# Kernel optimization log

Hardware: AMD Instinct MI355X
Metric: run time of the kernel (lower is better)

The kernel has to match this reference:

```python
import jax, jax.numpy as jnp
import numpy as np

N_HEAD = 12
LN_EPS = 1e-5


def setup_inputs() -> dict:
    key = jax.random.key(0)
    ks = jax.random.split(key, 4)
    B, T, C = 4, 2048, 768
    s = C ** -0.5
    return {
        "x": jax.random.normal(ks[0], (B, T, C), jnp.float32),
        "w_attn": jax.random.normal(ks[1], (C, 3 * C), jnp.float32) * s,
        "b_attn": jnp.zeros((3 * C,), jnp.float32),
        "w_proj": jax.random.normal(ks[2], (C, C), jnp.float32) * s,
        "b_proj": jnp.zeros((C,), jnp.float32),
        "ln1_g": jnp.ones((C,), jnp.float32),
        "ln1_b": jnp.zeros((C,), jnp.float32),
        "ln2_g": jnp.ones((C,), jnp.float32),
        "ln2_b": jnp.zeros((C,), jnp.float32),
    }


def _layernorm(x, g, b):
    mu = jnp.mean(x, axis=-1, keepdims=True)
    var = jnp.mean(jnp.square(x - mu), axis=-1, keepdims=True)
    return (x - mu) * jax.lax.rsqrt(var + LN_EPS) * g + b


def _attn(h, w_attn, b_attn, w_proj, b_proj):
    B, T, C = h.shape
    hd = C // N_HEAD
    # Faithful to torch: view(B,T,H,3*hd) then split 3*hd -> q,k,v per head
    qkv = (h @ w_attn + b_attn).reshape(B, T, N_HEAD, 3, hd)
    q = jnp.transpose(qkv[:, :, :, 0, :], (0, 2, 1, 3))  # (B,H,T,hd)
    k = jnp.transpose(qkv[:, :, :, 1, :], (0, 2, 1, 3))
    v = jnp.transpose(qkv[:, :, :, 2, :], (0, 2, 1, 3))
    # NOTE: scale is C**-0.5 (full embed dim) and there is NO causal mask,
    # exactly as in the source.
    scores = jnp.einsum("bhtd,bhsd->bhts", q, k) * (C ** -0.5)
    a = jax.nn.softmax(scores, axis=-1)
    y = jnp.einsum("bhts,bhsd->bhtd", a, v)
    y = jnp.transpose(y, (0, 2, 1, 3)).reshape(B, T, C)
    return y @ w_proj + b_proj


def reference(x, w_attn, b_attn, w_proj, b_proj, ln1_g, ln1_b, ln2_g, ln2_b):
    # Faithful to source Block.forward: attn applied twice, MLP never called.
    x = x + _attn(_layernorm(x, ln1_g, ln1_b), w_attn, b_attn, w_proj, b_proj)
    x = x + _attn(_layernorm(x, ln2_g, ln2_b), w_attn, b_attn, w_proj, b_proj)
    return x
```

## Files before the change

kernel.cpp:

```cpp
#include <hip/hip_runtime.h>


using bf16x8 = __attribute__((ext_vector_type(8))) short;
using f32x4  = __attribute__((ext_vector_type(4))) float;

__device__ __forceinline__ unsigned short f2b(float f) {
  unsigned u = __builtin_bit_cast(unsigned, f);
  u += 0x7FFFu + ((u >> 16) & 1u);
  return (unsigned short)(u >> 16);
}
__device__ __forceinline__ float b2f(unsigned short s) {
  return __builtin_bit_cast(float, (unsigned)s << 16);
}

#define ASYNC16(g, l)                                                        \
  __builtin_amdgcn_global_load_lds(                                          \
      (const __attribute__((address_space(1))) void*)(g),                    \
      (__attribute__((address_space(3))) void*)(l), 16, 0, 0)

__global__ __launch_bounds__(256) void wt_kernel(const float* __restrict__ w,
                                                 unsigned short* __restrict__ wt,
                                                 int N) {
  __shared__ float tile[32][33];
  const int n0 = blockIdx.x * 32, k0 = blockIdx.y * 32;
  const int tx = threadIdx.x, ty = threadIdx.y;
#pragma unroll
  for (int i = 0; i < 32; i += 8)
    tile[ty + i][tx] = w[(size_t)(k0 + ty + i) * N + n0 + tx];
  __syncthreads();
#pragma unroll
  for (int i = 0; i < 32; i += 8)
    wt[(size_t)(n0 + ty + i) * 768 + k0 + tx] = f2b(tile[tx][ty + i]);
}

__global__ __launch_bounds__(256) void ln_kernel(const float* __restrict__ x,
                                                 const float* __restrict__ g,
                                                 const float* __restrict__ b,
                                                 unsigned short* __restrict__ h) {
  __shared__ float red[8];
  const int row = blockIdx.x;
  const int tid = threadIdx.x;
  const float* xr = x + (size_t)row * 768;
  float v0 = xr[tid], v1 = xr[tid + 256], v2 = xr[tid + 512];
  float s = v0 + v1 + v2;
  float s2 = v0 * v0 + v1 * v1 + v2 * v2;
#pragma unroll
  for (int off = 1; off < 64; off <<= 1) {
    s += __shfl_xor(s, off);
    s2 += __shfl_xor(s2, off);
  }
  if ((tid & 63) == 0) { red[tid >> 6] = s; red[4 + (tid >> 6)] = s2; }
  __syncthreads();
  const float S  = red[0] + red[1] + red[2] + red[3];
  const float S2 = red[4] + red[5] + red[6] + red[7];
  const float mu  = S * (1.0f / 768.0f);
  const float var = S2 * (1.0f / 768.0f) - mu * mu;
  const float inv = rsqrtf(var + 1e-5f);
  unsigned short* hr = h + (size_t)row * 768;
  hr[tid]       = f2b((v0 - mu) * inv * g[tid] + b[tid]);
  hr[tid + 256] = f2b((v1 - mu) * inv * g[tid + 256] + b[tid + 256]);
  hr[tid + 512] = f2b((v2 - mu) * inv * g[tid + 512] + b[tid + 512]);
}

template <int EPI>
__global__ __launch_bounds__(256, 2) void gemm_kernel(
    const unsigned short* __restrict__ A, const unsigned short* __restrict__ Bt,
    const float* __restrict__ bias, const float* __restrict__ resid,
    unsigned short* __restrict__ q, unsigned short* __restrict__ k,
    unsigned short* __restrict__ vt, float* __restrict__ outF) {
  __shared__ alignas(16) unsigned short As[128 * 32];
  __shared__ alignas(16) unsigned short Bs[128 * 32];

  const int tid = threadIdx.x;
  const int wv = tid >> 6;
  const int lane = tid & 63;
  const int quad = lane >> 4;
  const int l15 = lane & 15;
  const int m0 = blockIdx.y * 128;
  const int n0 = blockIdx.x * 128;

  const int o0 = wv * 1024 + lane * 16;
  const int rT0 = o0 >> 6, c0 = (o0 & 63) >> 1;
  const int o1 = o0 + 4096;
  const int rT1 = o1 >> 6, c1 = (o1 & 63) >> 1;

  const unsigned short* gA0 = A + (size_t)(m0 + rT0) * 768 + c0;
  const unsigned short* gA1 = A + (size_t)(m0 + rT1) * 768 + c1;
  const unsigned short* gB0 = Bt + (size_t)(n0 + rT0) * 768 + c0;
  const unsigned short* gB1 = Bt + (size_t)(n0 + rT1) * 768 + c1;
  unsigned short* lA0 = &As[wv * 512];
  unsigned short* lA1 = &As[wv * 512 + 2048];
  unsigned short* lB0 = &Bs[wv * 512];
  unsigned short* lB1 = &Bs[wv * 512 + 2048];

  f32x4 acc[4][4];
#pragma unroll
  for (int i = 0; i < 4; ++i)
#pragma unroll
    for (int j = 0; j < 4; ++j) acc[i][j] = {0.f, 0.f, 0.f, 0.f};

  const int mBase = (wv >> 1) * 64;
  const int nBase = (wv & 1) * 64;

  for (int kk = 0; kk < 24; ++kk) {
    const int ko = kk * 32;
    ASYNC16(gA0 + ko, lA0);
    ASYNC16(gA1 + ko, lA1);
    ASYNC16(gB0 + ko, lB0);
    ASYNC16(gB1 + ko, lB1);
    __syncthreads();
    bf16x8 af[4], bfv[4];
#pragma unroll
    for (int mt = 0; mt < 4; ++mt)
      af[mt] = *(const bf16x8*)&As[(mBase + mt * 16 + l15) * 32 + quad * 8];
#pragma unroll
    for (int nt = 0; nt < 4; ++nt)
      bfv[nt] = *(const bf16x8*)&Bs[(nBase + nt * 16 + l15) * 32 + quad * 8];
#pragma unroll
    for (int mt = 0; mt < 4; ++mt)
#pragma unroll
      for (int nt = 0; nt < 4; ++nt)
        acc[mt][nt] = __builtin_amdgcn_mfma_f32_16x16x32_bf16(af[mt], bfv[nt],
                                                              acc[mt][nt], 0, 0, 0);
    __syncthreads();
  }

  if constexpr (EPI == 0) {
#pragma unroll
    for (int mt = 0; mt < 4; ++mt) {
#pragma unroll
      for (int nt = 0; nt < 4; ++nt) {
        const int n = n0 + nBase + nt * 16 + l15;
        const int head = n / 192;
        const int rem = n - head * 192;
        const int sel = rem >> 6;
        const int d = rem & 63;
        const float bv = bias[n];
#pragma unroll
        for (int r = 0; r < 4; ++r) {
          const int m = m0 + mBase + mt * 16 + quad * 4 + r;
          const int bb = m >> 11;
          const int t = m & 2047;
          const unsigned short val = f2b(acc[mt][nt][r] + bv);
          if (sel == 2) {
            vt[(((size_t)bb * 12 + head) * 64 + d) * 2048 + t] = val;
          } else {
            unsigned short* tgt = (sel == 0) ? q : k;
            tgt[(((size_t)bb * 12 + head) * 2048 + t) * 64 + d] = val;
          }
        }
      }
    }
  } else {
#pragma unroll
    for (int mt = 0; mt < 4; ++mt) {
#pragma unroll
      for (int nt = 0; nt < 4; ++nt) {
        const int n = n0 + nBase + nt * 16 + l15;
        const float bv = bias[n];
#pragma unroll
        for (int r = 0; r < 4; ++r) {
          const int m = m0 + mBase + mt * 16 + quad * 4 + r;
          const size_t idx = (size_t)m * 768 + n;
          outF[idx] = resid[idx] + bv + acc[mt][nt][r];
        }
      }
    }
  }
}

#define PAD 68
__global__ __launch_bounds__(256, 4) void attn_kernel(
    const unsigned short* __restrict__ Q, const unsigned short* __restrict__ Km,
    const unsigned short* __restrict__ Vt, unsigned short* __restrict__ Opart,
    float* __restrict__ lpart) {
  __shared__ alignas(16) unsigned short Ks[64 * PAD];
  __shared__ alignas(16) unsigned short Vs[64 * PAD];
  __shared__ alignas(16) unsigned short Ps[4][32 * PAD];

  const int bh = blockIdx.x;
  const int qt = blockIdx.y;
  const int split = blockIdx.z;
  const int tid = threadIdx.x;
  const int wv = tid >> 6;
  const int lane = tid & 63;
  const int quad = lane >> 4;
  const int l15 = lane & 15;
  const size_t bhT = (size_t)bh * 2048;

  bf16x8 qf[2][2];
#pragma unroll
  for (int mt = 0; mt < 2; ++mt) {
    const unsigned short* qb = Q + (bhT + qt * 128 + mt * 64 + wv * 16 + l15) * 64;
    qf[mt][0] = *(const bf16x8*)(qb + quad * 8);
    qf[mt][1] = *(const bf16x8*)(qb + 32 + quad * 8);
  }

  f32x4 o[2][4], ol[2];
#pragma unroll
  for (int mt = 0; mt < 2; ++mt) {
    ol[mt] = {0.f, 0.f, 0.f, 0.f};
#pragma unroll
    for (int nt = 0; nt < 4; ++nt) o[mt][nt] = {0.f, 0.f, 0.f, 0.f};
  }
  const bf16x8 ones = {0x3F80, 0x3F80, 0x3F80, 0x3F80,
                       0x3F80, 0x3F80, 0x3F80, 0x3F80};

  const int kr = tid >> 3;
  const int kc = (tid & 7) * 8;
  const unsigned short* gK = Km + (bhT + kr) * 64 + kc;
  const unsigned short* gV = Vt + ((size_t)bh * 64 + kr) * 2048 + kc;
  unsigned short* lK0 = &Ks[kr * PAD + kc];
  unsigned short* lK1 = &Ks[(kr + 32) * PAD + kc];
  unsigned short* lV0 = &Vs[kr * PAD + kc];
  unsigned short* lV1 = &Vs[(kr + 32) * PAD + kc];
  const float c2 = 0.052062786090587f;

  const int cBeg = split * 16, cEnd = cBeg + 16;
  bf16x8 sk0 = *(const bf16x8*)(gK + (size_t)cBeg * 4096);
  bf16x8 sk1 = *(const bf16x8*)(gK + (size_t)cBeg * 4096 + 2048);
  bf16x8 sv0 = *(const bf16x8*)(gV + cBeg * 64);
  bf16x8 sv1 = *(const bf16x8*)(gV + cBeg * 64 + 32 * 2048);

  for (int c = cBeg; c < cEnd; ++c) {
    *(bf16x8*)lK0 = sk0;
    *(bf16x8*)lK1 = sk1;
    *(bf16x8*)lV0 = sv0;
    *(bf16x8*)lV1 = sv1;
    __syncthreads();
    if (c + 1 < cEnd) {
      sk0 = *(const bf16x8*)(gK + (size_t)(c + 1) * 4096);
      sk1 = *(const bf16x8*)(gK + (size_t)(c + 1) * 4096 + 2048);
      sv0 = *(const bf16x8*)(gV + (c + 1) * 64);
      sv1 = *(const bf16x8*)(gV + (c + 1) * 64 + 32 * 2048);
    }

    f32x4 s[2][4];
#pragma unroll
    for (int nt = 0; nt < 4; ++nt) {
      s[0][nt] = {0.f, 0.f, 0.f, 0.f};
      s[1][nt] = {0.f, 0.f, 0.f, 0.f};
#pragma unroll
      for (int ks = 0; ks < 2; ++ks) {
        bf16x8 kf = *(const bf16x8*)&Ks[(nt * 16 + l15) * PAD + ks * 32 + quad * 8];
        s[0][nt] = __builtin_amdgcn_mfma_f32_16x16x32_bf16(qf[0][ks], kf, s[0][nt], 0, 0, 0);
        s[1][nt] = __builtin_amdgcn_mfma_f32_16x16x32_bf16(qf[1][ks], kf, s[1][nt], 0, 0, 0);
      }
    }

#pragma unroll
    for (int mt = 0; mt < 2; ++mt)
#pragma unroll
      for (int nt = 0; nt < 4; ++nt)
#pragma unroll
        for (int r = 0; r < 4; ++r) {
          const float p = __builtin_amdgcn_exp2f(s[mt][nt][r] * c2);
          Ps[wv][(mt * 16 + quad * 4 + r) * PAD + nt * 16 + l15] =
              (unsigned short)(__builtin_bit_cast(unsigned, p) >> 16);
        }

#pragma unroll
    for (int ks = 0; ks < 2; ++ks) {
      bf16x8 pf0 = *(const bf16x8*)&Ps[wv][(l15) * PAD + ks * 32 + quad * 8];
      bf16x8 pf1 = *(const bf16x8*)&Ps[wv][(16 + l15) * PAD + ks * 32 + quad * 8];
      ol[0] = __builtin_amdgcn_mfma_f32_16x16x32_bf16(pf0, ones, ol[0], 0, 0, 0);
      ol[1] = __builtin_amdgcn_mfma_f32_16x16x32_bf16(pf1, ones, ol[1], 0, 0, 0);
#pragma unroll
      for (int nt = 0; nt < 4; ++nt) {
        bf16x8 vf = *(const bf16x8*)&Vs[(nt * 16 + l15) * PAD + ks * 32 + quad * 8];
        o[0][nt] = __builtin_amdgcn_mfma_f32_16x16x32_bf16(pf0, vf, o[0][nt], 0, 0, 0);
        o[1][nt] = __builtin_amdgcn_mfma_f32_16x16x32_bf16(pf1, vf, o[1][nt], 0, 0, 0);
      }
    }
    __syncthreads();
  }

  unsigned short* Ob = Opart + ((size_t)split * 48 + bh) * 2048 * 64;
  float* lb = lpart + ((size_t)split * 48 + bh) * 2048;
#pragma unroll
  for (int mt = 0; mt < 2; ++mt) {
#pragma unroll
    for (int r = 0; r < 4; ++r) {
      const int t = qt * 128 + mt * 64 + wv * 16 + quad * 4 + r;
#pragma unroll
      for (int nt = 0; nt < 4; ++nt)
        Ob[(size_t)t * 64 + nt * 16 + l15] = f2b(o[mt][nt][r]);
      if (l15 == 0) lb[t] = ol[mt][r];
    }
  }
}

__global__ __launch_bounds__(256) void combine_kernel(
    const unsigned short* __restrict__ Opart, const float* __restrict__ lpart,
    unsigned short* __restrict__ Y) {
  const int bh = blockIdx.x;
  const int t = blockIdx.y * 256 + threadIdx.x;
  const int b = bh / 12;
  const int head = bh - b * 12;
  const size_t i0 = ((size_t)bh * 2048 + t) * 64;
  const size_t i1 = ((size_t)(48 + bh) * 2048 + t) * 64;
  const float l = lpart[(size_t)bh * 2048 + t] + lpart[(size_t)(48 + bh) * 2048 + t];
  const float rl = 1.0f / l;
  unsigned short* yb = Y + ((size_t)(b * 2048 + t)) * 768 + head * 64;
#pragma unroll
  for (int j = 0; j < 8; ++j) {
    bf16x8 a = *(const bf16x8*)(Opart + i0 + j * 8);
    bf16x8 c = *(const bf16x8*)(Opart + i1 + j * 8);
    bf16x8 r;
#pragma unroll
    for (int e = 0; e < 8; ++e) {
      const float v = (b2f((unsigned short)a[e]) + b2f((unsigned short)c[e])) * rl;
      r[e] = (short)f2b(v);
    }
    *(bf16x8*)(yb + j * 8) = r;
  }
}

extern "C" void kernel_launch(void* const* d_in, const int* in_sizes, int n_in,
                              void* d_out, int out_size, void* d_ws, size_t ws_size,
                              hipStream_t stream) {
  const float* x      = (const float*)d_in[0];
  const float* w_attn = (const float*)d_in[1];
  const float* b_attn = (const float*)d_in[2];
  const float* w_proj = (const float*)d_in[3];
  const float* b_proj = (const float*)d_in[4];
  const float* ln_g[2] = {(const float*)d_in[5], (const float*)d_in[7]};
  const float* ln_b[2] = {(const float*)d_in[6], (const float*)d_in[8]};
  float* out = (float*)d_out;

  unsigned short* wAt = (unsigned short*)d_ws;
  unsigned short* wPt = wAt + 2304 * 768;
  unsigned short* h   = wPt + 768 * 768;
  unsigned short* q   = h + 8192 * 768;
  unsigned short* k   = q + 48 * 2048 * 64;
  unsigned short* vt  = k + 48 * 2048 * 64;
  unsigned short* y   = vt + 48 * 2048 * 64;
  unsigned short* Op  = y + 8192 * 768;
  float* lp = (float*)(Op + 2 * 48 * 2048 * 64);

  wt_kernel<<<dim3(72, 24), dim3(32, 8), 0, stream>>>(w_attn, wAt, 2304);
  wt_kernel<<<dim3(24, 24), dim3(32, 8), 0, stream>>>(w_proj, wPt, 768);

  for (int pass = 0; pass < 2; ++pass) {
    const float* xin = pass ? (const float*)out : x;
    ln_kernel<<<8192, 256, 0, stream>>>(xin, ln_g[pass], ln_b[pass], h);
    gemm_kernel<0><<<dim3(18, 64), 256, 0, stream>>>(h, wAt, b_attn, nullptr,
                                                     q, k, vt, nullptr);
    attn_kernel<<<dim3(48, 16, 2), 256, 0, stream>>>(q, k, vt, Op, lp);
    combine_kernel<<<dim3(48, 8), 256, 0, stream>>>(Op, lp, y);
    gemm_kernel<1><<<dim3(6, 64), 256, 0, stream>>>(y, wPt, b_proj, xin,
                                                    nullptr, nullptr, nullptr, out);
  }
}
```

Measured before the change: 467.6 us.

## Transpose attention MFMA operands, stage output via LDS, move V transpose to separate kernel

The QKV GEMM epilogue now writes V in the same row-major layout as Q and K, and a new vtrans_kernel produces the transposed V that attention needs. The attention kernel swaps MFMA operand order so each lane holds four consecutive key scores for one query. That lets the probabilities be packed into 64-bit LDS stores, and the output tile is staged through shared memory so global writes are coalesced 16-byte vectors. The aim is to replace scattered 2-byte stores in the GEMM epilogue and attention output with contiguous ones. The cost is an extra kernel launch plus an extra read and write of V, and the new kernel's own transposed writes are still strided 2-byte stores.

```diff
diff --git a/kernel.cpp b/kernel.cpp
--- a/kernel.cpp
+++ b/kernel.cpp
@@ -67,7 +67,7 @@
     const unsigned short* __restrict__ A, const unsigned short* __restrict__ Bt,
     const float* __restrict__ bias, const float* __restrict__ resid,
     unsigned short* __restrict__ q, unsigned short* __restrict__ k,
-    unsigned short* __restrict__ vt, float* __restrict__ outF) {
+    unsigned short* __restrict__ v, float* __restrict__ outF) {
   __shared__ alignas(16) unsigned short As[128 * 32];
   __shared__ alignas(16) unsigned short Bs[128 * 32];
 
@@ -135,19 +135,15 @@
         const int rem = n - head * 192;
         const int sel = rem >> 6;
         const int d = rem & 63;
+        unsigned short* tgt = (sel == 0) ? q : (sel == 1) ? k : v;
         const float bv = bias[n];
 #pragma unroll
         for (int r = 0; r < 4; ++r) {
           const int m = m0 + mBase + mt * 16 + quad * 4 + r;
           const int bb = m >> 11;
           const int t = m & 2047;
-          const unsigned short val = f2b(acc[mt][nt][r] + bv);
-          if (sel == 2) {
-            vt[(((size_t)bb * 12 + head) * 64 + d) * 2048 + t] = val;
-          } else {
-            unsigned short* tgt = (sel == 0) ? q : k;
-            tgt[(((size_t)bb * 12 + head) * 2048 + t) * 64 + d] = val;
-          }
+          tgt[(((size_t)bb * 12 + head) * 2048 + t) * 64 + d] =
+              f2b(acc[mt][nt][r] + bv);
         }
       }
     }
@@ -169,14 +165,32 @@
   }
 }
 
-#define PAD 68
+__global__ __launch_bounds__(256) void vtrans_kernel(const unsigned short* __restrict__ V,
+                                                     unsigned short* __restrict__ Vt) {
+  const int bh = blockIdx.x;
+  const int t = blockIdx.y * 256 + threadIdx.x;
+  const uint4* s4 = (const uint4*)(V + ((size_t)bh * 2048 + t) * 64);
+  const size_t ob = (size_t)bh * 64 * 2048 + t;
+#pragma unroll
+  for (int i = 0; i < 8; ++i) {
+    const uint4 u = s4[i];
+    const unsigned w[4] = {u.x, u.y, u.z, u.w};
+#pragma unroll
+    for (int j = 0; j < 4; ++j) {
+      Vt[ob + (size_t)(i * 8 + j * 2) * 2048]     = (unsigned short)(w[j] & 0xFFFFu);
+      Vt[ob + (size_t)(i * 8 + j * 2 + 1) * 2048] = (unsigned short)(w[j] >> 16);
+    }
+  }
+}
+
+#define KP 68
 __global__ __launch_bounds__(256, 4) void attn_kernel(
     const unsigned short* __restrict__ Q, const unsigned short* __restrict__ Km,
     const unsigned short* __restrict__ Vt, unsigned short* __restrict__ Opart,
     float* __restrict__ lpart) {
-  __shared__ alignas(16) unsigned short Ks[64 * PAD];
-  __shared__ alignas(16) unsigned short Vs[64 * PAD];
-  __shared__ alignas(16) unsigned short Ps[4][32 * PAD];
+  __shared__ alignas(16) unsigned short SM[64 * KP * 2 + 4 * 32 * KP];
+  unsigned short* Ks = SM;
+  unsigned short* Vs = SM + 64 * KP;
 
   const int bh = blockIdx.x;
   const int qt = blockIdx.y;
@@ -187,22 +201,23 @@
   const int quad = lane >> 4;
   const int l15 = lane & 15;
   const size_t bhT = (size_t)bh * 2048;
+  unsigned short* Pw = SM + 2 * 64 * KP + wv * 32 * KP;
 
   bf16x8 qf[2][2];
 #pragma unroll
-  for (int mt = 0; mt < 2; ++mt) {
-    const unsigned short* qb = Q + (bhT + qt * 128 + mt * 64 + wv * 16 + l15) * 64;
-    qf[mt][0] = *(const bf16x8*)(qb + quad * 8);
-    qf[mt][1] = *(const bf16x8*)(qb + 32 + quad * 8);
-  }
-
-  f32x4 o[2][4], ol[2];
-#pragma unroll
-  for (int mt = 0; mt < 2; ++mt) {
-    ol[mt] = {0.f, 0.f, 0.f, 0.f};
-#pragma unroll
-    for (int nt = 0; nt < 4; ++nt) o[mt][nt] = {0.f, 0.f, 0.f, 0.f};
-  }
+  for (int qt2 = 0; qt2 < 2; ++qt2) {
+    const unsigned short* qb = Q + (bhT + qt * 128 + wv * 32 + qt2 * 16 + l15) * 64;
+    qf[qt2][0] = *(const bf16x8*)(qb + quad * 8);
+    qf[qt2][1] = *(const bf16x8*)(qb + 32 + quad * 8);
+  }
+
+  f32x4 o[4][2], ol[2];
+#pragma unroll
+  for (int dt = 0; dt < 4; ++dt)
+#pragma unroll
+    for (int qt2 = 0; qt2 < 2; ++qt2) o[dt][qt2] = {0.f, 0.f, 0.f, 0.f};
+  ol[0] = {0.f, 0.f, 0.f, 0.f};
+  ol[1] = {0.f, 0.f, 0.f, 0.f};
   const bf16x8 ones = {0x3F80, 0x3F80, 0x3F80, 0x3F80,
                        0x3F80, 0x3F80, 0x3F80, 0x3F80};
 
@@ -210,10 +225,10 @@
   const int kc = (tid & 7) * 8;
   const unsigned short* gK = Km + (bhT + kr) * 64 + kc;
   const unsigned short* gV = Vt + ((size_t)bh * 64 + kr) * 2048 + kc;
-  unsigned short* lK0 = &Ks[kr * PAD + kc];
-  unsigned short* lK1 = &Ks[(kr + 32) * PAD + kc];
-  unsigned short* lV0 = &Vs[kr * PAD + kc];
-  unsigned short* lV1 = &Vs[(kr + 32) * PAD + kc];
+  unsigned short* lK0 = &Ks[kr * KP + kc];
+  unsigned short* lK1 = &Ks[(kr + 32) * KP + kc];
+  unsigned short* lV0 = &Vs[kr * KP + kc];
+  unsigned short* lV1 = &Vs[(kr + 32) * KP + kc];
   const float c2 = 0.052062786090587f;
 
   const int cBeg = split * 16, cEnd = cBeg + 16;
@@ -235,58 +250,69 @@
       sv1 = *(const bf16x8*)(gV + (c + 1) * 64 + 32 * 2048);
     }
 
-    f32x4 s[2][4];
-#pragma unroll
-    for (int nt = 0; nt < 4; ++nt) {
-      s[0][nt] = {0.f, 0.f, 0.f, 0.f};
-      s[1][nt] = {0.f, 0.f, 0.f, 0.f};
-#pragma unroll
-      for (int ks = 0; ks < 2; ++ks) {
-        bf16x8 kf = *(const bf16x8*)&Ks[(nt * 16 + l15) * PAD + ks * 32 + quad * 8];
-        s[0][nt] = __builtin_amdgcn_mfma_f32_16x16x32_bf16(qf[0][ks], kf, s[0][nt], 0, 0, 0);
-        s[1][nt] = __builtin_amdgcn_mfma_f32_16x16x32_bf16(qf[1][ks], kf, s[1][nt], 0, 0, 0);
+#pragma unroll
+    for (int tt = 0; tt < 4; ++tt) {
+      bf16x8 kf0 = *(const bf16x8*)&Ks[(tt * 16 + l15) * KP + quad * 8];
+      bf16x8 kf1 = *(const bf16x8*)&Ks[(tt * 16 + l15) * KP + 32 + quad * 8];
+      f32x4 s0 = {0.f, 0.f, 0.f, 0.f}, s1 = {0.f, 0.f, 0.f, 0.f};
+      s0 = __builtin_amdgcn_mfma_f32_16x16x32_bf16(kf0, qf[0][0], s0, 0, 0, 0);
+      s0 = __builtin_amdgcn_mfma_f32_16x16x32_bf16(kf1, qf[0][1], s0, 0, 0, 0);
+      s1 = __builtin_amdgcn_mfma_f32_16x16x32_bf16(kf0, qf[1][0], s1, 0, 0, 0);
+      s1 = __builtin_amdgcn_mfma_f32_16x16x32_bf16(kf1, qf[1][1], s1, 0, 0, 0);
+      unsigned long long pk0 = 0, pk1 = 0;
+#pragma unroll
+      for (int r = 0; r < 4; ++r) {
+        const unsigned p0 = __builtin_bit_cast(
+            unsigned, __builtin_amdgcn_exp2f(s0[r] * c2)) >> 16;
+        const unsigned p1 = __builtin_bit_cast(
+            unsigned, __builtin_amdgcn_exp2f(s1[r] * c2)) >> 16;
+        pk0 |= (unsigned long long)p0 << (16 * r);
+        pk1 |= (unsigned long long)p1 << (16 * r);
       }
-    }
-
-#pragma unroll
-    for (int mt = 0; mt < 2; ++mt)
-#pragma unroll
-      for (int nt = 0; nt < 4; ++nt)
-#pragma unroll
-        for (int r = 0; r < 4; ++r) {
-          const float p = __builtin_amdgcn_exp2f(s[mt][nt][r] * c2);
-          Ps[wv][(mt * 16 + quad * 4 + r) * PAD + nt * 16 + l15] =
-              (unsigned short)(__builtin_bit_cast(unsigned, p) >> 16);
-        }
+      *(unsigned long long*)&Pw[l15 * KP + tt * 16 + quad * 4] = pk0;
+      *(unsigned long long*)&Pw[(16 + l15) * KP + tt * 16 + quad * 4] = pk1;
+    }
 
 #pragma unroll
     for (int ks = 0; ks < 2; ++ks) {
-      bf16x8 pf0 = *(const bf16x8*)&Ps[wv][(l15) * PAD + ks * 32 + quad * 8];
-      bf16x8 pf1 = *(const bf16x8*)&Ps[wv][(16 + l15) * PAD + ks * 32 + quad * 8];
-      ol[0] = __builtin_amdgcn_mfma_f32_16x16x32_bf16(pf0, ones, ol[0], 0, 0, 0);
-      ol[1] = __builtin_amdgcn_mfma_f32_16x16x32_bf16(pf1, ones, ol[1], 0, 0, 0);
-#pragma unroll
-      for (int nt = 0; nt < 4; ++nt) {
-        bf16x8 vf = *(const bf16x8*)&Vs[(nt * 16 + l15) * PAD + ks * 32 + quad * 8];
-        o[0][nt] = __builtin_amdgcn_mfma_f32_16x16x32_bf16(pf0, vf, o[0][nt], 0, 0, 0);
-        o[1][nt] = __builtin_amdgcn_mfma_f32_16x16x32_bf16(pf1, vf, o[1][nt], 0, 0, 0);
+      bf16x8 pf0 = *(const bf16x8*)&Pw[l15 * KP + ks * 32 + quad * 8];
+      bf16x8 pf1 = *(const bf16x8*)&Pw[(16 + l15) * KP + ks * 32 + quad * 8];
+      ol[0] = __builtin_amdgcn_mfma_f32_16x16x32_bf16(ones, pf0, ol[0], 0, 0, 0);
+      ol[1] = __builtin_amdgcn_mfma_f32_16x16x32_bf16(ones, pf1, ol[1], 0, 0, 0);
+#pragma unroll
+      for (int dt = 0; dt < 4; ++dt) {
+        bf16x8 vf = *(const bf16x8*)&Vs[(dt * 16 + l15) * KP + ks * 32 + quad * 8];
+        o[dt][0] = __builtin_amdgcn_mfma_f32_16x16x32_bf16(vf, pf0, o[dt][0], 0, 0, 0);
+        o[dt][1] = __builtin_amdgcn_mfma_f32_16x16x32_bf16(vf, pf1, o[dt][1], 0, 0, 0);
       }
     }
     __syncthreads();
   }
 
-  unsigned short* Ob = Opart + ((size_t)split * 48 + bh) * 2048 * 64;
-  float* lb = lpart + ((size_t)split * 48 + bh) * 2048;
-#pragma unroll
-  for (int mt = 0; mt < 2; ++mt) {
-#pragma unroll
-    for (int r = 0; r < 4; ++r) {
-      const int t = qt * 128 + mt * 64 + wv * 16 + quad * 4 + r;
-#pragma unroll
-      for (int nt = 0; nt < 4; ++nt)
-        Ob[(size_t)t * 64 + nt * 16 + l15] = f2b(o[mt][nt][r]);
-      if (l15 == 0) lb[t] = ol[mt][r];
-    }
+  unsigned short* T = SM;
+#pragma unroll
+  for (int qt2 = 0; qt2 < 2; ++qt2) {
+    const int trow = wv * 32 + qt2 * 16 + l15;
+#pragma unroll
+    for (int dt = 0; dt < 4; ++dt) {
+      unsigned long long pk = 0;
+#pragma unroll
+      for (int r = 0; r < 4; ++r)
+        pk |= (unsigned long long)f2b(o[dt][qt2][r]) << (16 * r);
+      *(unsigned long long*)&T[trow * KP + dt * 16 + quad * 4] = pk;
+    }
+    if (quad == 0)
+      lpart[((size_t)split * 48 + bh) * 2048 + qt * 128 + trow] = ol[qt2][0];
+  }
+  __syncthreads();
+  {
+    const int tr = tid >> 1;
+    const int dc = (tid & 1) * 32;
+    unsigned short* Ob =
+        Opart + (((size_t)split * 48 + bh) * 2048 + qt * 128 + tr) * 64 + dc;
+#pragma unroll
+    for (int i = 0; i < 4; ++i)
+      *(bf16x8*)(Ob + i * 8) = *(const bf16x8*)&T[tr * KP + dc + i * 8];
   }
 }
 
@@ -333,7 +359,8 @@
   unsigned short* h   = wPt + 768 * 768;
   unsigned short* q   = h + 8192 * 768;
   unsigned short* k   = q + 48 * 2048 * 64;
-  unsigned short* vt  = k + 48 * 2048 * 64;
+  unsigned short* v   = k + 48 * 2048 * 64;
+  unsigned short* vt  = v + 48 * 2048 * 64;
   unsigned short* y   = vt + 48 * 2048 * 64;
   unsigned short* Op  = y + 8192 * 768;
   float* lp = (float*)(Op + 2 * 48 * 2048 * 64);
@@ -345,7 +372,8 @@
     const float* xin = pass ? (const float*)out : x;
     ln_kernel<<<8192, 256, 0, stream>>>(xin, ln_g[pass], ln_b[pass], h);
     gemm_kernel<0><<<dim3(18, 64), 256, 0, stream>>>(h, wAt, b_attn, nullptr,
-                                                     q, k, vt, nullptr);
+                                                     q, k, v, nullptr);
+    vtrans_kernel<<<dim3(48, 8), 256, 0, stream>>>(v, vt);
     attn_kernel<<<dim3(48, 16, 2), 256, 0, stream>>>(q, k, vt, Op, lp);
     combine_kernel<<<dim3(48, 8), 256, 0, stream>>>(Op, lp, y);
     gemm_kernel<1><<<dim3(6, 64), 256, 0, stream>>>(y, wPt, b_proj, xin,
```

Measured after the change: 783.0 us. +67.4%, slower.
